# Kernel optimization log

Hardware: AMD Instinct MI355X
Metric: run time of the kernel (lower is better)

The kernel has to match this reference:

```python
import jax, jax.numpy as jnp
import numpy as np

N_CUST = 500000
N_FUND = 50000
N_EDGE = 4000000
D_CUST = 101
D_FUND = 1
HID = 64


def setup_inputs() -> dict:
    key = jax.random.key(0)
    ks = jax.random.split(key, 16)
    s = lambda fan_in: 1.0 / np.sqrt(fan_in)
    return {
        "x_customer": jax.random.normal(ks[0], (N_CUST, D_CUST), jnp.float32),
        "x_fund": jax.random.normal(ks[1], (N_FUND, D_FUND), jnp.float32),
        "src_fund": jax.random.randint(ks[2], (N_EDGE,), 0, N_FUND, jnp.int64),
        "dst_customer": jax.random.randint(ks[3], (N_EDGE,), 0, N_CUST, jnp.int64),
        # per-node-type input projections
        "W_cust": jax.random.uniform(ks[4], (D_CUST, HID), jnp.float32, -s(D_CUST), s(D_CUST)),
        "b_cust": jax.random.uniform(ks[5], (HID,), jnp.float32, -s(D_CUST), s(D_CUST)),
        "W_fund": jax.random.uniform(ks[6], (D_FUND, HID), jnp.float32, -s(D_FUND), s(D_FUND)),
        "b_fund": jax.random.uniform(ks[7], (HID,), jnp.float32, -s(D_FUND), s(D_FUND)),
        # SAGEConv fund->customer: lin_l (neighbor aggr, bias) + lin_r (self, no bias)
        "W_l": jax.random.uniform(ks[8], (HID, HID), jnp.float32, -s(HID), s(HID)),
        "b_l": jax.random.uniform(ks[9], (HID,), jnp.float32, -s(HID), s(HID)),
        "W_r": jax.random.uniform(ks[10], (HID, HID), jnp.float32, -s(HID), s(HID)),
        # output head
        "W_out": jax.random.uniform(ks[11], (HID, 2), jnp.float32, -s(HID), s(HID)),
        "b_out": jax.random.uniform(ks[12], (2,), jnp.float32, -s(HID), s(HID)),
    }


def reference(x_customer, x_fund, src_fund, dst_customer,
              W_cust, b_cust, W_fund, b_fund, W_l, b_l, W_r, W_out, b_out):
    # per-node-type linear + relu
    h_c = jax.nn.relu(x_customer @ W_cust + b_cust)  # [N_CUST, HID]
    h_f = jax.nn.relu(x_fund @ W_fund + b_fund)      # [N_FUND, HID]

    # SAGEConv (fund -> customer): gather src fund features per edge,
    # mean-aggregate by destination customer (scatter-sum / count)
    msgs = h_f[src_fund]  # [N_EDGE, HID]
    summed = jax.ops.segment_sum(msgs, dst_customer, num_segments=N_CUST)
    cnt = jax.ops.segment_sum(jnp.ones((msgs.shape[0],), msgs.dtype),
                              dst_customer, num_segments=N_CUST)
    mean = summed / jnp.maximum(cnt, 1.0)[:, None]

    out_c = mean @ W_l + b_l + h_c @ W_r  # SAGE: lin_l(aggr) + lin_r(self)
    return out_c @ W_out + b_out          # [N_CUST, 2]
```

## Files before the change

### kernel.cpp

```cpp
#include <hip/hip_runtime.h>
#include <stdint.h>

#define N_CUST 500000
#define N_FUND 50000
#define N_EDGE 4000000
#define D_CUST 101
#define HID 64

#define NB   512
#define EPB  ((N_EDGE + NB - 1) / NB)
#define CB   512
#define NBKT ((N_CUST + CB - 1) / CB)
#define CAP  5120

#define GEMM_GRID 2048

typedef float float4u __attribute__((ext_vector_type(4), aligned(4)));
using frag_ab = __attribute__((ext_vector_type(8))) short;
using frag_cd = __attribute__((ext_vector_type(4))) float;

struct __align__(16) Accum { float g0, g1, cnt, pad; };

__device__ __forceinline__ short f2bf(float f) {
    unsigned u = __float_as_uint(f);
    u += 0x7fffu + ((u >> 16) & 1u);
    return (short)(u >> 16);
}

__global__ __launch_bounds__(256) void k_gf(
    const float* __restrict__ x_fund,
    const float* __restrict__ W_fund,
    const float* __restrict__ b_fund,
    const float* __restrict__ W_l,
    const float* __restrict__ W_r,
    const float* __restrict__ W_out,
    const float* __restrict__ Wc,
    const float* __restrict__ b_l,
    const float* __restrict__ b_out,
    float2* __restrict__ gf,
    frag_ab* __restrict__ wcb,
    float* __restrict__ Bt,
    float* __restrict__ c2,
    unsigned* __restrict__ gcur,
    float4* __restrict__ Az)
{
    __shared__ float sAf[128];
    __shared__ float sWf[64];
    __shared__ float sBf[64];
    int t = threadIdx.x;

    if (Az != nullptr) {
        float4 z4 = make_float4(0.f, 0.f, 0.f, 0.f);
        for (int i = blockIdx.x * 256 + t; i < N_CUST; i += gridDim.x * 256)
            Az[i] = z4;
    }

    if (t < 128) {
        int h = t >> 1, j = t & 1;
        float s = 0.f;
        for (int k = 0; k < 64; ++k)
            s = fmaf(W_l[h * 64 + k], W_out[k * 2 + j], s);
        sAf[t] = s;
    } else if (t < 192) {
        sWf[t - 128] = W_fund[t - 128];
    } else {
        sBf[t - 192] = b_fund[t - 192];
    }
    __syncthreads();

    int f = blockIdx.x * 256 + t;
    if (f < N_FUND) {
        float xf = x_fund[f];
        float g0 = 0.f, g1 = 0.f;
        #pragma unroll
        for (int h = 0; h < 64; ++h) {
            float hf = fmaxf(fmaf(xf, sWf[h], sBf[h]), 0.f);
            g0 = fmaf(hf, sAf[2 * h + 0], g0);
            g1 = fmaf(hf, sAf[2 * h + 1], g1);
        }
        gf[f] = make_float2(g0, g1);
    }

    if (blockIdx.x == 0) {
        for (int k = t; k < NBKT; k += 256) gcur[k] = 0u;
        if (t < 128) {
            int h = t >> 1, j = t & 1;
            float s = 0.f;
            for (int k = 0; k < 64; ++k)
                s = fmaf(W_r[h * 64 + k], W_out[k * 2 + j], s);
            Bt[t] = s;
        } else if (t < 130) {
            int j = t - 128;
            float s = b_out[j];
            for (int k = 0; k < 64; ++k)
                s = fmaf(b_l[k], W_out[k * 2 + j], s);
            c2[j] = s;
        }
        for (int sidx = t; sidx < 1024; sidx += 256) {
            int fidx = sidx >> 6, l = sidx & 63;
            int c = l & 15, q = l >> 4;
            int nt = fidx >> 2, kc = fidx & 3;
            frag_ab fr;
            #pragma unroll
            for (int j = 0; j < 8; ++j) {
                int kk = kc * 32 + q * 8 + j;
                int h  = nt * 16 + c;
                fr[j] = (kk < D_CUST) ? f2bf(Wc[kk * HID + h]) : (short)0;
            }
            wcb[sidx] = fr;
        }
    }
}

__global__ __launch_bounds__(256) void k_reorder(
    const int* __restrict__ src, const int* __restrict__ dst,
    unsigned* __restrict__ gcur, unsigned* __restrict__ recs)
{
    __shared__ unsigned hist[NBKT];
    __shared__ unsigned localOff[NBKT];
    __shared__ unsigned cur[NBKT];
    __shared__ unsigned baseG[NBKT];
    __shared__ unsigned ldsRec[EPB];
    __shared__ unsigned short ldsBkt[EPB];

    int t = threadIdx.x, b = blockIdx.x;
    int e0 = b * EPB, e1 = min(e0 + EPB, N_EDGE);
    int cntE = e1 - e0;

    for (int k = t; k < NBKT; k += 256) hist[k] = 0;
    __syncthreads();
    for (int e = e0 + t; e < e1; e += 256)
        atomicAdd(&hist[((unsigned)dst[e]) >> 9], 1u);
    __syncthreads();

    if (t < 64) {
        unsigned v[16], pre[16], run = 0;
        #pragma unroll
        for (int j = 0; j < 16; ++j) {
            int idx = t * 16 + j;
            v[j] = (idx < NBKT) ? hist[idx] : 0u;
            pre[j] = run; run += v[j];
        }
        unsigned sc = run;
        #pragma unroll
        for (int d = 1; d < 64; d <<= 1) {
            unsigned n = __shfl_up(sc, d, 64);
            if (t >= d) sc += n;
        }
        unsigned lane_excl = sc - run;
        #pragma unroll
        for (int j = 0; j < 16; ++j) {
            int idx = t * 16 + j;
            if (idx < NBKT) {
                localOff[idx] = lane_excl + pre[j];
                cur[idx]      = lane_excl + pre[j];
            }
        }
    }
    __syncthreads();

    for (int k = t; k < NBKT; k += 256) {
        unsigned h = hist[k];
        baseG[k] = h ? ((unsigned)k * CAP + atomicAdd(&gcur[k], h)) : 0u;
    }

    for (int e = e0 + t; e < e1; e += 256) {
        unsigned d = (unsigned)dst[e];
        unsigned s = (unsigned)src[e];
        unsigned k = d >> 9;
        unsigned p = atomicAdd(&cur[k], 1u);
        ldsRec[p] = s | ((d & 511u) << 16);
        ldsBkt[p] = (unsigned short)k;
    }
    __syncthreads();

    for (int i = t; i < cntE; i += 256) {
        unsigned k = ldsBkt[i];
        unsigned g = baseG[k] + (i - localOff[k]);
        if (g < (k + 1u) * CAP) recs[g] = ldsRec[i];
    }
}

__global__ __launch_bounds__(256) void k_agg(
    const unsigned* __restrict__ recs, const unsigned* __restrict__ gcur,
    const float2* __restrict__ gf, float2* __restrict__ mean2)
{
    __shared__ float s0[CB], s1[CB], scn[CB];
    int t = threadIdx.x, k = blockIdx.x;

    for (int c = t; c < CB; c += 256) { s0[c] = 0.f; s1[c] = 0.f; scn[c] = 0.f; }
    __syncthreads();

    unsigned n = min(gcur[k], (unsigned)CAP);
    unsigned r0 = (unsigned)k * CAP;
    for (unsigned i = r0 + t; i < r0 + n; i += 256) {
        unsigned r = recs[i];
        float2 g = gf[r & 0xFFFFu];
        unsigned dl = r >> 16;
        atomicAdd(&s0[dl], g.x);
        atomicAdd(&s1[dl], g.y);
        atomicAdd(&scn[dl], 1.f);
    }
    __syncthreads();

    int cust0 = k * CB;
    for (int c = t; c < CB; c += 256) {
        int row = cust0 + c;
        if (row < N_CUST) {
            float inv = 1.0f / fmaxf(scn[c], 1.0f);
            mean2[row] = make_float2(s0[c] * inv, s1[c] * inv);
        }
    }
}

__global__ __launch_bounds__(256) void k_gemm(
    const float* __restrict__ x, const float* __restrict__ bc,
    const frag_ab* __restrict__ wcb, const float* __restrict__ Bt,
    const float* __restrict__ c2, const float2* __restrict__ mean2,
    float2* __restrict__ out)
{
    __shared__ float sBt[128];
    __shared__ float zb[4][16 * 68];

    int t = threadIdx.x;
    int w = t >> 6, lane = t & 63;
    int c = lane & 15, q = lane >> 4;
    float* z = zb[w];

    if (t < 128) sBt[t] = Bt[t];
    frag_ab bfrag[16];
    #pragma unroll
    for (int f = 0; f < 16; ++f) bfrag[f] = wcb[f * 64 + lane];
    float bcv[4];
    #pragma unroll
    for (int nt = 0; nt < 4; ++nt) bcv[nt] = bc[nt * 16 + c];
    float c20 = c2[0], c21 = c2[1];
    __syncthreads();

    const int NT = N_CUST / 16;
    for (int tl = blockIdx.x * 4 + w; tl < NT; tl += gridDim.x * 4) {
        int row0 = tl * 16;
        const float* xr = x + (size_t)(row0 + c) * D_CUST;
        frag_ab af[4];
        #pragma unroll
        for (int kc = 0; kc < 3; ++kc) {
            float4u lo = *(const float4u*)(xr + kc * 32 + q * 8);
            float4u hi = *(const float4u*)(xr + kc * 32 + q * 8 + 4);
            frag_ab f;
            f[0]=f2bf(lo[0]); f[1]=f2bf(lo[1]); f[2]=f2bf(lo[2]); f[3]=f2bf(lo[3]);
            f[4]=f2bf(hi[0]); f[5]=f2bf(hi[1]); f[6]=f2bf(hi[2]); f[7]=f2bf(hi[3]);
            af[kc] = f;
        }
        {
            frag_ab f = {0,0,0,0,0,0,0,0};
            if (q == 0) {
                float4u lo = *(const float4u*)(xr + 96);
                f[0]=f2bf(lo[0]); f[1]=f2bf(lo[1]); f[2]=f2bf(lo[2]); f[3]=f2bf(lo[3]);
                f[4]=f2bf(xr[100]);
            }
            af[3] = f;
        }
        frag_cd acc[4];
        #pragma unroll
        for (int nt = 0; nt < 4; ++nt)
            acc[nt] = (frag_cd){bcv[nt], bcv[nt], bcv[nt], bcv[nt]};
        #pragma unroll
        for (int kc = 0; kc < 4; ++kc)
            #pragma unroll
            for (int nt = 0; nt < 4; ++nt)
                acc[nt] = __builtin_amdgcn_mfma_f32_16x16x32_bf16(
                    af[kc], bfrag[nt * 4 + kc], acc[nt], 0, 0, 0);

        #pragma unroll
        for (int nt = 0; nt < 4; ++nt)
            #pragma unroll
            for (int i = 0; i < 4; ++i)
                z[(q * 4 + i) * 68 + nt * 16 + c] = fmaxf(acc[nt][i], 0.f);

        float p0 = 0.f, p1 = 0.f;
        #pragma unroll
        for (int j4 = 0; j4 < 4; ++j4) {
            float4u zv = *(const float4u*)(z + c * 68 + q * 16 + j4 * 4);
            float4u b0 = *(const float4u*)(sBt + q * 32 + j4 * 8);
            float4u b1 = *(const float4u*)(sBt + q * 32 + j4 * 8 + 4);
            p0 = fmaf(zv[0], b0[0], p0); p1 = fmaf(zv[0], b0[1], p1);
            p0 = fmaf(zv[1], b0[2], p0); p1 = fmaf(zv[1], b0[3], p1);
            p0 = fmaf(zv[2], b1[0], p0); p1 = fmaf(zv[2], b1[1], p1);
            p0 = fmaf(zv[3], b1[2], p0); p1 = fmaf(zv[3], b1[3], p1);
        }
        p0 += __shfl_xor(p0, 16, 64); p0 += __shfl_xor(p0, 32, 64);
        p1 += __shfl_xor(p1, 16, 64); p1 += __shfl_xor(p1, 32, 64);
        if (q == 0) {
            float2 m = mean2[row0 + c];
            out[row0 + c] = make_float2(p0 + c20 + m.x, p1 + c21 + m.y);
        }
    }
}

__global__ __launch_bounds__(256) void k_scatter_direct(
    const int* __restrict__ src, const int* __restrict__ dst,
    const float2* __restrict__ gf, Accum* __restrict__ A)
{
    int stride = gridDim.x * 256;
    for (int e = blockIdx.x * 256 + threadIdx.x; e < N_EDGE; e += stride) {
        int s = src[e], d = dst[e];
        float2 g = gf[s];
        unsafeAtomicAdd(&A[d].g0, g.x);
        unsafeAtomicAdd(&A[d].g1, g.y);
        unsafeAtomicAdd(&A[d].cnt, 1.0f);
    }
}

__global__ __launch_bounds__(256) void k_mean(
    const Accum* __restrict__ A, float2* __restrict__ mean2)
{
    int i = blockIdx.x * 256 + threadIdx.x;
    if (i < N_CUST) {
        Accum a = A[i];
        float inv = 1.0f / fmaxf(a.cnt, 1.0f);
        mean2[i] = make_float2(a.g0 * inv, a.g1 * inv);
    }
}

extern "C" void kernel_launch(void* const* d_in, const int* in_sizes, int n_in,
                              void* d_out, int out_size, void* d_ws, size_t ws_size,
                              hipStream_t stream) {
    const float* x_customer = (const float*)d_in[0];
    const float* x_fund     = (const float*)d_in[1];
    const int*   src_fund   = (const int*)d_in[2];
    const int*   dst_cust   = (const int*)d_in[3];
    const float* W_cust     = (const float*)d_in[4];
    const float* b_cust     = (const float*)d_in[5];
    const float* W_fund     = (const float*)d_in[6];
    const float* b_fund     = (const float*)d_in[7];
    const float* W_l        = (const float*)d_in[8];
    const float* b_l        = (const float*)d_in[9];
    const float* W_r        = (const float*)d_in[10];
    const float* W_out      = (const float*)d_in[11];
    const float* b_out      = (const float*)d_in[12];

    char* ws = (char*)d_ws;
    const size_t NEED_FAST = 24429780ull;

    if (ws_size >= NEED_FAST) {
        unsigned* recs = (unsigned*)(ws);
        float2*   gf   = (float2*)  (ws + 20008960);
        float2*   mn2  = (float2*)  (ws + 20408960);
        frag_ab*  wcb  = (frag_ab*) (ws + 24408960);
        float*    Bt   = (float*)   (ws + 24425344);
        float*    c2   = (float*)   (ws + 24425856);
        unsigned* gcur = (unsigned*)(ws + 24425872);

        k_gf<<<256, 256, 0, stream>>>(
            x_fund, W_fund, b_fund, W_l, W_r, W_out, W_cust, b_l, b_out,
            gf, wcb, Bt, c2, gcur, nullptr);
        k_reorder<<<NB, 256, 0, stream>>>(src_fund, dst_cust, gcur, recs);
        k_agg<<<NBKT, 256, 0, stream>>>(recs, gcur, gf, mn2);
        k_gemm<<<GEMM_GRID, 256, 0, stream>>>(
            x_customer, b_cust, wcb, Bt, c2, mn2, (float2*)d_out);
    } else {
        Accum*    A    = (Accum*)   (ws);
        float2*   mn2  = (float2*)  (ws + 8000000);
        float2*   gf   = (float2*)  (ws + 12000000);
        frag_ab*  wcb  = (frag_ab*) (ws + 12400000);
        float*    Bt   = (float*)   (ws + 12416384);
        float*    c2   = (float*)   (ws + 12416896);
        unsigned* gcur = (unsigned*)(ws + 12416912);

        k_gf<<<256, 256, 0, stream>>>(
            x_fund, W_fund, b_fund, W_l, W_r, W_out, W_cust, b_l, b_out,
            gf, wcb, Bt, c2, gcur, (float4*)A);
        k_scatter_direct<<<2048, 256, 0, stream>>>(src_fund, dst_cust, gf, A);
        k_mean<<<(N_CUST + 255) / 256, 256, 0, stream>>>(A, mn2);
        k_gemm<<<GEMM_GRID, 256, 0, stream>>>(
            x_customer, b_cust, wcb, Bt, c2, mn2, (float2*)d_out);
    }
}
```

Before: 457.6 us.

## Fuse bucket aggregation with customer GEMM and pad bucket counters

Merges the per-bucket mean aggregation into the customer projection GEMM, so each 512-customer block accumulates its edge messages in LDS and then computes its rows' MLP output directly. This removes the mean2 round trip through global memory and one kernel launch. The global bucket counters are padded to separate cache lines to cut atomic contention. The reorder write-out now walks each bucket contiguously per thread instead of per edge, which drops the ldsBkt array but leaves the work per thread serial and uneven. The fused kernel has a fixed grid of about 977 blocks of 512 threads, which may give less parallelism for the GEMM part than the old 2048-block grid.

```diff
diff --git a/kernel.cpp b/kernel.cpp
--- a/kernel.cpp
+++ b/kernel.cpp
@@ -12,8 +12,7 @@
 #define CB   512
 #define NBKT ((N_CUST + CB - 1) / CB)
 #define CAP  5120
-
-#define GEMM_GRID 2048
+#define GPAD 32
 
 typedef float float4u __attribute__((ext_vector_type(4), aligned(4)));
 using frag_ab = __attribute__((ext_vector_type(8))) short;
@@ -82,7 +81,7 @@
     }
 
     if (blockIdx.x == 0) {
-        for (int k = t; k < NBKT; k += 256) gcur[k] = 0u;
+        for (int k = t; k < NBKT * GPAD; k += 256) gcur[k] = 0u;
         if (t < 128) {
             int h = t >> 1, j = t & 1;
             float s = 0.f;
@@ -121,11 +120,9 @@
     __shared__ unsigned cur[NBKT];
     __shared__ unsigned baseG[NBKT];
     __shared__ unsigned ldsRec[EPB];
-    __shared__ unsigned short ldsBkt[EPB];
 
     int t = threadIdx.x, b = blockIdx.x;
     int e0 = b * EPB, e1 = min(e0 + EPB, N_EDGE);
-    int cntE = e1 - e0;
 
     for (int k = t; k < NBKT; k += 256) hist[k] = 0;
     __syncthreads();
@@ -161,7 +158,7 @@
 
     for (int k = t; k < NBKT; k += 256) {
         unsigned h = hist[k];
-        baseG[k] = h ? ((unsigned)k * CAP + atomicAdd(&gcur[k], h)) : 0u;
+        baseG[k] = h ? ((unsigned)k * CAP + atomicAdd(&gcur[k * GPAD], h)) : 0u;
     }
 
     for (int e = e0 + t; e < e1; e += 256) {
@@ -170,30 +167,42 @@
         unsigned k = d >> 9;
         unsigned p = atomicAdd(&cur[k], 1u);
         ldsRec[p] = s | ((d & 511u) << 16);
-        ldsBkt[p] = (unsigned short)k;
-    }
-    __syncthreads();
-
-    for (int i = t; i < cntE; i += 256) {
-        unsigned k = ldsBkt[i];
-        unsigned g = baseG[k] + (i - localOff[k]);
-        if (g < (k + 1u) * CAP) recs[g] = ldsRec[i];
-    }
-}
-
-__global__ __launch_bounds__(256) void k_agg(
+    }
+    __syncthreads();
+
+    for (int k = t; k < NBKT; k += 256) {
+        unsigned i0 = localOff[k], i1 = cur[k];
+        unsigned g = baseG[k];
+        unsigned gend = ((unsigned)k + 1u) * CAP;
+        for (unsigned i = i0; i < i1 && g < gend; ++i, ++g)
+            recs[g] = ldsRec[i];
+    }
+}
+
+__global__ __launch_bounds__(512) void k_bucket(
     const unsigned* __restrict__ recs, const unsigned* __restrict__ gcur,
-    const float2* __restrict__ gf, float2* __restrict__ mean2)
+    const float2* __restrict__ gf,
+    const float* __restrict__ x, const float* __restrict__ bc,
+    const frag_ab* __restrict__ wcb, const float* __restrict__ Bt,
+    const float* __restrict__ c2,
+    float2* __restrict__ out)
 {
     __shared__ float s0[CB], s1[CB], scn[CB];
+    __shared__ float sBt[128];
+    __shared__ float zb[8][16 * 68];
+
     int t = threadIdx.x, k = blockIdx.x;
-
-    for (int c = t; c < CB; c += 256) { s0[c] = 0.f; s1[c] = 0.f; scn[c] = 0.f; }
-    __syncthreads();
-
-    unsigned n = min(gcur[k], (unsigned)CAP);
+    int w = t >> 6, lane = t & 63;
+    int c = lane & 15, q = lane >> 4;
+    float* z = zb[w];
+
+    if (t < 128) sBt[t] = Bt[t];
+    for (int cc = t; cc < CB; cc += 512) { s0[cc] = 0.f; s1[cc] = 0.f; scn[cc] = 0.f; }
+    __syncthreads();
+
+    unsigned n = min(gcur[(unsigned)k * GPAD], (unsigned)CAP);
     unsigned r0 = (unsigned)k * CAP;
-    for (unsigned i = r0 + t; i < r0 + n; i += 256) {
+    for (unsigned i = r0 + t; i < r0 + n; i += 512) {
         unsigned r = recs[i];
         float2 g = gf[r & 0xFFFFu];
         unsigned dl = r >> 16;
@@ -201,15 +210,102 @@
         atomicAdd(&s1[dl], g.y);
         atomicAdd(&scn[dl], 1.f);
     }
+
+    frag_ab bfrag[16];
+    #pragma unroll
+    for (int f = 0; f < 16; ++f) bfrag[f] = wcb[f * 64 + lane];
+    float bcv[4];
+    #pragma unroll
+    for (int nt = 0; nt < 4; ++nt) bcv[nt] = bc[nt * 16 + c];
+    float c20 = c2[0], c21 = c2[1];
     __syncthreads();
 
     int cust0 = k * CB;
-    for (int c = t; c < CB; c += 256) {
-        int row = cust0 + c;
-        if (row < N_CUST) {
-            float inv = 1.0f / fmaxf(scn[c], 1.0f);
-            mean2[row] = make_float2(s0[c] * inv, s1[c] * inv);
-        }
+    int n_tiles = min(CB / 16, (N_CUST - cust0) >> 4);
+
+    for (int tl = w; tl < n_tiles; tl += 8) {
+        int lrow = tl * 16 + c;
+        int row = cust0 + lrow;
+        const float* xr = x + (size_t)row * D_CUST;
+        frag_ab af[4];
+        #pragma unroll
+        for (int kc = 0; kc < 3; ++kc) {
+            float4u lo = *(const float4u*)(xr + kc * 32 + q * 8);
+            float4u hi = *(const float4u*)(xr + kc * 32 + q * 8 + 4);
+            frag_ab f;
+            f[0]=f2bf(lo[0]); f[1]=f2bf(lo[1]); f[2]=f2bf(lo[2]); f[3]=f2bf(lo[3]);
+            f[4]=f2bf(hi[0]); f[5]=f2bf(hi[1]); f[6]=f2bf(hi[2]); f[7]=f2bf(hi[3]);
+            af[kc] = f;
+        }
+        {
+            frag_ab f = {0,0,0,0,0,0,0,0};
+            if (q == 0) {
+                float4u lo = *(const float4u*)(xr + 96);
+                f[0]=f2bf(lo[0]); f[1]=f2bf(lo[1]); f[2]=f2bf(lo[2]); f[3]=f2bf(lo[3]);
+                f[4]=f2bf(xr[100]);
+            }
+            af[3] = f;
+        }
+        frag_cd acc[4];
+        #pragma unroll
+        for (int nt = 0; nt < 4; ++nt)
+            acc[nt] = (frag_cd){bcv[nt], bcv[nt], bcv[nt], bcv[nt]};
+        #pragma unroll
+        for (int kc = 0; kc < 4; ++kc)
+            #pragma unroll
+            for (int nt = 0; nt < 4; ++nt)
+                acc[nt] = __builtin_amdgcn_mfma_f32_16x16x32_bf16(
+                    af[kc], bfrag[nt * 4 + kc], acc[nt], 0, 0, 0);
+
+        #pragma unroll
+        for (int nt = 0; nt < 4; ++nt)
+            #pragma unroll
+            for (int i = 0; i < 4; ++i)
+                z[(q * 4 + i) * 68 + nt * 16 + c] = fmaxf(acc[nt][i], 0.f);
+
+        float p0 = 0.f, p1 = 0.f;
+        #pragma unroll
+        for (int j4 = 0; j4 < 4; ++j4) {
+            float4u zv = *(const float4u*)(z + c * 68 + q * 16 + j4 * 4);
+            float4u b0 = *(const float4u*)(sBt + q * 32 + j4 * 8);
+            float4u b1 = *(const float4u*)(sBt + q * 32 + j4 * 8 + 4);
+            p0 = fmaf(zv[0], b0[0], p0); p1 = fmaf(zv[0], b0[1], p1);
+            p0 = fmaf(zv[1], b0[2], p0); p1 = fmaf(zv[1], b0[3], p1);
+            p0 = fmaf(zv[2], b1[0], p0); p1 = fmaf(zv[2], b1[1], p1);
+            p0 = fmaf(zv[3], b1[2], p0); p1 = fmaf(zv[3], b1[3], p1);
+        }
+        p0 += __shfl_xor(p0, 16, 64); p0 += __shfl_xor(p0, 32, 64);
+        p1 += __shfl_xor(p1, 16, 64); p1 += __shfl_xor(p1, 32, 64);
+        if (q == 0) {
+            float inv = 1.0f / fmaxf(scn[lrow], 1.0f);
+            out[row] = make_float2(fmaf(s0[lrow], inv, p0 + c20),
+                                   fmaf(s1[lrow], inv, p1 + c21));
+        }
+    }
+}
+
+__global__ __launch_bounds__(256) void k_scatter_direct(
+    const int* __restrict__ src, const int* __restrict__ dst,
+    const float2* __restrict__ gf, Accum* __restrict__ A)
+{
+    int stride = gridDim.x * 256;
+    for (int e = blockIdx.x * 256 + threadIdx.x; e < N_EDGE; e += stride) {
+        int s = src[e], d = dst[e];
+        float2 g = gf[s];
+        unsafeAtomicAdd(&A[d].g0, g.x);
+        unsafeAtomicAdd(&A[d].g1, g.y);
+        unsafeAtomicAdd(&A[d].cnt, 1.0f);
+    }
+}
+
+__global__ __launch_bounds__(256) void k_mean(
+    const Accum* __restrict__ A, float2* __restrict__ mean2)
+{
+    int i = blockIdx.x * 256 + threadIdx.x;
+    if (i < N_CUST) {
+        Accum a = A[i];
+        float inv = 1.0f / fmaxf(a.cnt, 1.0f);
+        mean2[i] = make_float2(a.g0 * inv, a.g1 * inv);
     }
 }
 
@@ -270,13 +366,11 @@
             for (int nt = 0; nt < 4; ++nt)
                 acc[nt] = __builtin_amdgcn_mfma_f32_16x16x32_bf16(
                     af[kc], bfrag[nt * 4 + kc], acc[nt], 0, 0, 0);
-
         #pragma unroll
         for (int nt = 0; nt < 4; ++nt)
             #pragma unroll
             for (int i = 0; i < 4; ++i)
                 z[(q * 4 + i) * 68 + nt * 16 + c] = fmaxf(acc[nt][i], 0.f);
-
         float p0 = 0.f, p1 = 0.f;
         #pragma unroll
         for (int j4 = 0; j4 < 4; ++j4) {
@@ -294,31 +388,6 @@
             float2 m = mean2[row0 + c];
             out[row0 + c] = make_float2(p0 + c20 + m.x, p1 + c21 + m.y);
         }
-    }
-}
-
-__global__ __launch_bounds__(256) void k_scatter_direct(
-    const int* __restrict__ src, const int* __restrict__ dst,
-    const float2* __restrict__ gf, Accum* __restrict__ A)
-{
-    int stride = gridDim.x * 256;
-    for (int e = blockIdx.x * 256 + threadIdx.x; e < N_EDGE; e += stride) {
-        int s = src[e], d = dst[e];
-        float2 g = gf[s];
-        unsafeAtomicAdd(&A[d].g0, g.x);
-        unsafeAtomicAdd(&A[d].g1, g.y);
-        unsafeAtomicAdd(&A[d].cnt, 1.0f);
-    }
-}
-
-__global__ __launch_bounds__(256) void k_mean(
-    const Accum* __restrict__ A, float2* __restrict__ mean2)
-{
-    int i = blockIdx.x * 256 + threadIdx.x;
-    if (i < N_CUST) {
-        Accum a = A[i];
-        float inv = 1.0f / fmaxf(a.cnt, 1.0f);
-        mean2[i] = make_float2(a.g0 * inv, a.g1 * inv);
     }
 }
 
@@ -340,24 +409,22 @@
     const float* b_out      = (const float*)d_in[12];
 
     char* ws = (char*)d_ws;
-    const size_t NEED_FAST = 24429780ull;
+    const size_t NEED_FAST = 20550976ull;
 
     if (ws_size >= NEED_FAST) {
         unsigned* recs = (unsigned*)(ws);
         float2*   gf   = (float2*)  (ws + 20008960);
-        float2*   mn2  = (float2*)  (ws + 20408960);
-        frag_ab*  wcb  = (frag_ab*) (ws + 24408960);
-        float*    Bt   = (float*)   (ws + 24425344);
-        float*    c2   = (float*)   (ws + 24425856);
-        unsigned* gcur = (unsigned*)(ws + 24425872);
+        frag_ab*  wcb  = (frag_ab*) (ws + 20408960);
+        float*    Bt   = (float*)   (ws + 20425344);
+        float*    c2   = (float*)   (ws + 20425856);
+        unsigned* gcur = (unsigned*)(ws + 20425920);
 
         k_gf<<<256, 256, 0, stream>>>(
             x_fund, W_fund, b_fund, W_l, W_r, W_out, W_cust, b_l, b_out,
             gf, wcb, Bt, c2, gcur, nullptr);
         k_reorder<<<NB, 256, 0, stream>>>(src_fund, dst_cust, gcur, recs);
-        k_agg<<<NBKT, 256, 0, stream>>>(recs, gcur, gf, mn2);
-        k_gemm<<<GEMM_GRID, 256, 0, stream>>>(
-            x_customer, b_cust, wcb, Bt, c2, mn2, (float2*)d_out);
+        k_bucket<<<NBKT, 512, 0, stream>>>(
+            recs, gcur, gf, x_customer, b_cust, wcb, Bt, c2, (float2*)d_out);
     } else {
         Accum*    A    = (Accum*)   (ws);
         float2*   mn2  = (float2*)  (ws + 8000000);
@@ -365,14 +432,14 @@
         frag_ab*  wcb  = (frag_ab*) (ws + 12400000);
         float*    Bt   = (float*)   (ws + 12416384);
         float*    c2   = (float*)   (ws + 12416896);
-        unsigned* gcur = (unsigned*)(ws + 12416912);
+        unsigned* gcur = (unsigned*)(ws + 12416960);
 
         k_gf<<<256, 256, 0, stream>>>(
             x_fund, W_fund, b_fund, W_l, W_r, W_out, W_cust, b_l, b_out,
             gf, wcb, Bt, c2, gcur, (float4*)A);
         k_scatter_direct<<<2048, 256, 0, stream>>>(src_fund, dst_cust, gf, A);
         k_mean<<<(N_CUST + 255) / 256, 256, 0, stream>>>(A, mn2);
-        k_gemm<<<GEMM_GRID, 256, 0, stream>>>(
+        k_gemm<<<2048, 256, 0, stream>>>(
             x_customer, b_cust, wcb, Bt, c2, mn2, (float2*)d_out);
     }
 }
```

Result: no change. 459.7 us (+0.4%).
